# Kernel optimization log

Hardware: AMD Instinct MI355X
Metric: run time of the kernel (lower is better)

The kernel has to match this reference:

```python
import jax, jax.numpy as jnp
import numpy as np

N_NODES = 100000
N_EDGES = 1600000
N_FEAT = 128
HIDDEN = 64
NUM_GRAPHS = 64


def setup_inputs() -> dict:
    key = jax.random.key(0)
    ks = jax.random.split(key, 10)
    x = jax.random.normal(ks[0], (N_NODES, N_FEAT), dtype=jnp.float32)
    W = jax.random.normal(ks[1], (N_FEAT, HIDDEN), dtype=jnp.float32) * (1.0 / np.sqrt(N_FEAT))
    b = jax.random.normal(ks[2], (HIDDEN,), dtype=jnp.float32) * 0.01
    W1 = jax.random.normal(ks[3], (HIDDEN, 16), dtype=jnp.float32) * (1.0 / np.sqrt(HIDDEN))
    b1 = jax.random.normal(ks[4], (16,), dtype=jnp.float32) * 0.01
    W2 = jax.random.normal(ks[5], (16, 1), dtype=jnp.float32) * 0.25
    b2 = jax.random.normal(ks[6], (1,), dtype=jnp.float32) * 0.01
    edge_index = jax.random.randint(ks[7], (2, N_EDGES), 0, N_NODES, dtype=jnp.int64)
    batch = jnp.sort(jax.random.randint(ks[8], (N_NODES,), 0, NUM_GRAPHS, dtype=jnp.int64))
    return {"x": x, "W": W, "b": b, "W1": W1, "b1": b1, "W2": W2, "b2": b2,
            "edge_index": edge_index, "batch": batch, "num_graphs": NUM_GRAPHS}


def reference(x, W, b, W1, b1, W2, b2, edge_index, batch, num_graphs):
    N = x.shape[0]
    # GCNConv: h = D^-1/2 (A + I) D^-1/2 (x W) + b
    h = x @ W  # [N, H]
    loops = jnp.arange(N, dtype=edge_index.dtype)
    src = jnp.concatenate([edge_index[0], loops])  # source nodes (with self-loops)
    dst = jnp.concatenate([edge_index[1], loops])  # target nodes
    deg = jax.ops.segment_sum(jnp.ones(dst.shape, h.dtype), dst, num_segments=N)
    dis = jnp.where(deg > 0, jax.lax.rsqrt(deg), 0.0)  # deg^-1/2, 0 for isolated
    norm = dis[src] * dis[dst]  # [E+N]
    msg = h[src] * norm[:, None]  # gather + normalize
    agg = jax.ops.segment_sum(msg, dst, num_segments=N) + b  # scatter-add + bias
    hn = jax.nn.relu(agg)
    # global_add_pool over graphs
    u = jax.ops.segment_sum(hn, batch, num_segments=num_graphs)  # [G, H]
    out = jax.nn.relu(u @ W1 + b1) @ W2 + b2  # [G, 1]
    return out.reshape(-1)
```

## Files before the change

kernel.cpp:

```cpp
#include <hip/hip_runtime.h>

#define N_NODES   100000
#define N_FEAT    128
#define N_EDGES   1600000
#define HIDDEN    64
#define NUM_GRAPHS 64
#define CHUNK   4096
#define NCHUNK  ((N_EDGES + CHUNK - 1) / CHUNK)
#define BSHIFT  8
#define NBUCKET ((N_NODES + 255) >> 8)
#define OFFS_W  (NBUCKET + 1)
#define CAP     4800
#define QE      ((CAP + 511) / 512)
#define WT_BLOCKS 4
#define GEMM_GRID ((N_NODES + 127) / 128)
#define AGG_NODES 64
#define AGG_BLOCKS ((N_NODES + AGG_NODES - 1) / AGG_NODES)

typedef unsigned int  uint32;
typedef unsigned short ushort16;

typedef __attribute__((ext_vector_type(8))) __bf16 bf16x8;
typedef __attribute__((ext_vector_type(4))) float  f32x4;
union Frag8 { bf16x8 v; unsigned short s[8]; uint4 q; };

static __device__ __forceinline__ unsigned short f2bf(float f) {
    uint32 u = __float_as_uint(f);
    u += 0x7fffu + ((u >> 16) & 1u);
    return (unsigned short)(u >> 16);
}

static __device__ __forceinline__ int scan512(int v, int t, int* wsum) {
    const int lane = t & 63;
    const int wv   = t >> 6;
#pragma unroll
    for (int off = 1; off < 64; off <<= 1) {
        const int n = __shfl_up(v, off);
        if (lane >= off) v += n;
    }
    if (lane == 63) wsum[wv] = v;
    __syncthreads();
    if (t < 8) {
        int s = wsum[t];
#pragma unroll
        for (int off = 1; off < 8; off <<= 1) {
            const int n = __shfl_up(s, off);
            if (t >= off) s += n;
        }
        wsum[t] = s;
    }
    __syncthreads();
    if (wv > 0) v += wsum[wv - 1];
    return v;
}

static __device__ __forceinline__ int scan256(int v, int t, int* wsum) {
    const int lane = t & 63;
    const int wv   = t >> 6;
#pragma unroll
    for (int off = 1; off < 64; off <<= 1) {
        const int n = __shfl_up(v, off);
        if (lane >= off) v += n;
    }
    if (lane == 63 && wv < 4) wsum[wv] = v;
    __syncthreads();
    if (t < 4) {
        int s = wsum[t];
#pragma unroll
        for (int off = 1; off < 4; off <<= 1) {
            const int n = __shfl_up(s, off);
            if (t >= off) s += n;
        }
        wsum[t] = s;
    }
    __syncthreads();
    if (wv > 0 && wv < 4) v += wsum[wv - 1];
    return v;
}

__global__ __launch_bounds__(512) void k_pre(const float* __restrict__ W,
                                             ushort16* __restrict__ Wt,
                                             const int* __restrict__ ei,
                                             int* __restrict__ src_out,
                                             unsigned char* __restrict__ dst8,
                                             int* __restrict__ offs) {
    __shared__ int hist[512];
    __shared__ int excl[512];
    __shared__ int wsum[8];
    __shared__ int ssrc[CHUNK];
    __shared__ int sdst[CHUNK];

    if (blockIdx.x < WT_BLOCKS) {
        const int base = blockIdx.x * 2048 + threadIdx.x;
#pragma unroll
        for (int j = 0; j < 4; ++j) {
            const int idx = base + j * 512;
            const int k = idx >> 6, n = idx & 63;
            Wt[n * N_FEAT + k] = f2bf(W[idx]);
        }
        return;
    }

    const int c = blockIdx.x - WT_BLOCKS;
    const int base = c * CHUNK;
    const int n = min(CHUNK, N_EDGES - base);
    const int t = threadIdx.x;
    hist[t] = 0;
    __syncthreads();

    int es[CHUNK / 512], ed[CHUNK / 512], rk[CHUNK / 512];
#pragma unroll
    for (int k = 0; k < CHUNK / 512; ++k) {
        const int i = t + k * 512;
        if (i < n) {
            ed[k] = __builtin_nontemporal_load(&ei[N_EDGES + base + i]);
            es[k] = __builtin_nontemporal_load(&ei[base + i]);
            rk[k] = atomicAdd(&hist[ed[k] >> BSHIFT], 1);
        }
    }
    __syncthreads();

    const int cnt = hist[t];
    const int inc = scan512(cnt, t, wsum);
    excl[t] = inc - cnt;
    __syncthreads();
    if (t <= NBUCKET) offs[c * OFFS_W + t] = base + excl[t];

#pragma unroll
    for (int k = 0; k < CHUNK / 512; ++k) {
        const int i = t + k * 512;
        if (i < n) {
            const int pos = excl[ed[k] >> BSHIFT] + rk[k];
            ssrc[pos] = es[k];
            sdst[pos] = ed[k];
        }
    }
    __syncthreads();

    for (int i = t; i < n; i += 512)
        src_out[base + i] = ssrc[i];
    for (int i = t * 4; i < n; i += 2048) {
        const uint32 p = (uint32)(sdst[i] & 255)
                       | ((uint32)(sdst[i + 1] & 255) << 8)
                       | ((uint32)(sdst[i + 2] & 255) << 16)
                       | ((uint32)(sdst[i + 3] & 255) << 24);
        *(uint32*)&dst8[base + i] = p;
    }
}

__global__ __launch_bounds__(512) void k_mix(const float* __restrict__ x,
                                             const ushort16* __restrict__ Wt,
                                             ushort16* __restrict__ hb,
                                             const int* __restrict__ offs,
                                             const int* __restrict__ src_tmp,
                                             const unsigned char* __restrict__ dst8,
                                             int* __restrict__ srcs,
                                             int* __restrict__ row_ptr,
                                             int* __restrict__ row_end,
                                             float* __restrict__ dis) {
    __shared__ int hist[256];
    __shared__ int nxt[256];
    __shared__ int segb[NCHUNK];
    __shared__ int pre[NCHUNK + 1];
    __shared__ unsigned short cmap[CAP];
    __shared__ int ssrc[CAP];
    __shared__ int wsum[8];
    __shared__ int sb;

    if (blockIdx.x >= NBUCKET) {
        const int t    = threadIdx.x;
        const int lane = t & 63;
        const int wv   = t >> 6;
        const int m15  = lane & 15;
        const int quad = lane >> 4;
        const int base = (blockIdx.x - NBUCKET) * 128 + wv * 16;
        const int arow = min(base + m15, N_NODES - 1);

        const float* xr = &x[(size_t)arow * N_FEAT + quad * 8];
        float4 xa[4][2];
#pragma unroll
        for (int kc = 0; kc < 4; ++kc) {
            xa[kc][0] = *(const float4*)&xr[kc * 32];
            xa[kc][1] = *(const float4*)&xr[kc * 32 + 4];
        }

        Frag8 bfr[4][4];
#pragma unroll
        for (int nt = 0; nt < 4; ++nt) {
            const ushort16* wr = &Wt[(nt * 16 + m15) * N_FEAT + quad * 8];
#pragma unroll
            for (int kc = 0; kc < 4; ++kc)
                bfr[nt][kc].q = *(const uint4*)&wr[kc * 32];
        }

        Frag8 af[4];
#pragma unroll
        for (int kc = 0; kc < 4; ++kc) {
            const float* f = (const float*)&xa[kc][0];
#pragma unroll
            for (int j = 0; j < 8; ++j) af[kc].s[j] = f2bf(f[j]);
        }

        f32x4 acc[4];
#pragma unroll
        for (int nt = 0; nt < 4; ++nt) acc[nt] = (f32x4){0.f, 0.f, 0.f, 0.f};

#pragma unroll
        for (int kc = 0; kc < 4; ++kc)
#pragma unroll
            for (int nt = 0; nt < 4; ++nt)
                acc[nt] = __builtin_amdgcn_mfma_f32_16x16x32_bf16(af[kc].v, bfr[nt][kc].v,
                                                                  acc[nt], 0, 0, 0);

#pragma unroll
        for (int r = 0; r < 4; ++r) {
            const int orow = base + quad * 4 + r;
            if (orow < N_NODES) {
#pragma unroll
                for (int nt = 0; nt < 4; ++nt)
                    hb[(size_t)orow * HIDDEN + nt * 16 + m15] = f2bf(acc[nt][r]);
            }
        }
        return;
    }

    const int b = blockIdx.x;
    const int lo = b << BSHIFT;
    const int t = threadIdx.x;

    if (t < 256) hist[t] = 0;
    if (t == 0) sb = 0;
    __syncthreads();

    int len = 0;
    if (t < NCHUNK) {
        const int s0 = offs[t * OFFS_W + b];
        const int s1 = offs[t * OFFS_W + b + 1];
        segb[t] = s0;
        len = s1 - s0;
        atomicAdd(&sb, s0 - t * CHUNK);
    }
    const int inc = scan512(len, t, wsum);
    if (t == 0) pre[0] = 0;
    if (t < NCHUNK) pre[t + 1] = inc;
    __syncthreads();

    const int total  = pre[NCHUNK];
    const int bstart = sb;
    const bool fits  = (total <= CAP);

    int es[QE], ed[QE], rk[QE];
    if (fits) {
        if (t < NCHUNK) {
            const int p0 = pre[t], p1 = pre[t + 1];
            for (int j = p0; j < p1; ++j) cmap[j] = (unsigned short)t;
        }
        __syncthreads();
#pragma unroll
        for (int q = 0; q < QE; ++q) {
            const int e = t + q * 512;
            if (e < total) {
                const int c2 = cmap[e];
                const int gidx = segb[c2] + (e - pre[c2]);
                ed[q] = dst8[gidx];
                es[q] = src_tmp[gidx];
                rk[q] = atomicAdd(&hist[ed[q]], 1);
            }
        }
    } else {
        const int lane = t & 63, wv = t >> 6;
        for (int c2 = wv; c2 < NCHUNK; c2 += 8)
            for (int i = segb[c2] + lane; i < segb[c2] + (pre[c2 + 1] - pre[c2]); i += 64)
                atomicAdd(&hist[dst8[i]], 1);
    }
    __syncthreads();

    const int cv  = (t < 256) ? hist[t] : 0;
    const int hin = scan256(cv, t, wsum);
    if (t < 256) {
        const int excl = hin - cv;
        nxt[t] = excl;
        const int node = lo + t;
        if (node < N_NODES) {
            row_ptr[node] = bstart + excl;
            row_end[node] = bstart + excl + cv;
            dis[node]     = rsqrtf((float)cv + 1.0f);
        }
    }
    __syncthreads();

    if (fits) {
#pragma unroll
        for (int q = 0; q < QE; ++q)
            if (t + q * 512 < total) ssrc[nxt[ed[q]] + rk[q]] = es[q];
        __syncthreads();
        for (int i = t; i < total; i += 512)
            srcs[bstart + i] = ssrc[i];
    } else {
        const int lane = t & 63, wv = t >> 6;
        for (int c2 = wv; c2 < NCHUNK; c2 += 8)
            for (int i = segb[c2] + lane; i < segb[c2] + (pre[c2 + 1] - pre[c2]); i += 64) {
                const int d = dst8[i];
                const int pos = atomicAdd(&nxt[d], 1);
                srcs[bstart + pos] = src_tmp[i];
            }
    }
}

__global__ __launch_bounds__(256) void k_agg(const int* __restrict__ rp_g,
                                             const int* __restrict__ re_g,
                                             const int* __restrict__ srcs,
                                             const ushort16* __restrict__ hb,
                                             const float* __restrict__ dis,
                                             const float* __restrict__ bias,
                                             const int* __restrict__ batch,
                                             float* __restrict__ u) {
    __shared__ float sp[AGG_NODES * 65];
    __shared__ int   rp[AGG_NODES];
    __shared__ int   rc[AGG_NODES];
    __shared__ float sdn[AGG_NODES];
    __shared__ int   gbs[AGG_NODES];
    const int b  = blockIdx.x;
    const int lo = b * AGG_NODES;
    const int t  = threadIdx.x;

    if (t < AGG_NODES) {
        const int node = lo + t;
        const bool ok = node < N_NODES;
        const int p = ok ? rp_g[node] : 0;
        rp[t]  = p;
        rc[t]  = ok ? (re_g[node] - p) : 0;
        sdn[t] = ok ? dis[node] : 0.f;
        gbs[t] = ok ? batch[node] : 0;
    }
    __syncthreads();

    const int lane = t & 63;
    const int k    = lane & 7;
    const int kb   = lane & 56;
    const int grp  = (t >> 6) * 8 + (lane >> 3);

    float acc[2][8];
#pragma unroll
    for (int a = 0; a < 2; ++a)
#pragma unroll
        for (int j = 0; j < 8; ++j) acc[a][j] = 0.f;

#pragma unroll
    for (int a = 0; a < 2; ++a) {
        const int n   = grp * 2 + a;
        const int beg = rp[n];
        const int L   = rc[n];
        for (int i = 0; i < L; i += 8) {
            const int idx = beg + min(i + k, L - 1);
            const int sv  = srcs[idx];
            const float wv_ = dis[sv];
            uint4 v[8];
            float w[8];
#pragma unroll
            for (int j = 0; j < 8; ++j) {
                const int sj = __shfl(sv, kb | j);
                w[j] = __shfl(wv_, kb | j);
                v[j] = *(const uint4*)&hb[(size_t)sj * HIDDEN + k * 8];
            }
            const int rem = L - i;
#pragma unroll
            for (int j = 0; j < 8; ++j) {
                const float m = (j < rem) ? w[j] : 0.f;
                acc[a][0] = fmaf(__uint_as_float(v[j].x << 16),         m, acc[a][0]);
                acc[a][1] = fmaf(__uint_as_float(v[j].x & 0xffff0000u), m, acc[a][1]);
                acc[a][2] = fmaf(__uint_as_float(v[j].y << 16),         m, acc[a][2]);
                acc[a][3] = fmaf(__uint_as_float(v[j].y & 0xffff0000u), m, acc[a][3]);
                acc[a][4] = fmaf(__uint_as_float(v[j].z << 16),         m, acc[a][4]);
                acc[a][5] = fmaf(__uint_as_float(v[j].z & 0xffff0000u), m, acc[a][5]);
                acc[a][6] = fmaf(__uint_as_float(v[j].w << 16),         m, acc[a][6]);
                acc[a][7] = fmaf(__uint_as_float(v[j].w & 0xffff0000u), m, acc[a][7]);
            }
        }
    }

    const float4 b0 = *(const float4*)&bias[k * 8];
    const float4 b1 = *(const float4*)&bias[k * 8 + 4];
#pragma unroll
    for (int a = 0; a < 2; ++a) {
        const int n = grp * 2 + a;
        const uint4 hv = *(const uint4*)
            &hb[(size_t)min(lo + n, N_NODES - 1) * HIDDEN + k * 8];
        const float dn = sdn[n];
        float4 r0, r1;
        r0.x = fmaxf(fmaf(fmaf(__uint_as_float(hv.x << 16),         dn, acc[a][0]), dn, b0.x), 0.f);
        r0.y = fmaxf(fmaf(fmaf(__uint_as_float(hv.x & 0xffff0000u), dn, acc[a][1]), dn, b0.y), 0.f);
        r0.z = fmaxf(fmaf(fmaf(__uint_as_float(hv.y << 16),         dn, acc[a][2]), dn, b0.z), 0.f);
        r0.w = fmaxf(fmaf(fmaf(__uint_as_float(hv.y & 0xffff0000u), dn, acc[a][3]), dn, b0.w), 0.f);
        r1.x = fmaxf(fmaf(fmaf(__uint_as_float(hv.z << 16),         dn, acc[a][4]), dn, b1.x), 0.f);
        r1.y = fmaxf(fmaf(fmaf(__uint_as_float(hv.z & 0xffff0000u), dn, acc[a][5]), dn, b1.y), 0.f);
        r1.z = fmaxf(fmaf(fmaf(__uint_as_float(hv.w << 16),         dn, acc[a][6]), dn, b1.z), 0.f);
        r1.w = fmaxf(fmaf(fmaf(__uint_as_float(hv.w & 0xffff0000u), dn, acc[a][7]), dn, b1.w), 0.f);
        *(float4*)&sp[n * 65 + k * 8]     = r0;
        *(float4*)&sp[n * 65 + k * 8 + 4] = r1;
    }
    __syncthreads();

    const int f   = t & 63;
    const int seg = t >> 6;
    float a_ = 0.f;
    int   cg = -1;
    for (int n2 = seg * 16; n2 < seg * 16 + 16; ++n2) {
        const int node = lo + n2;
        if (node >= N_NODES) break;
        const float r = sp[n2 * 65 + f];
        const int gr = gbs[n2];
        if (gr != cg) {
            if (cg >= 0) atomicAdd(&u[cg * HIDDEN + f], a_);
            cg = gr; a_ = r;
        } else {
            a_ += r;
        }
    }
    if (cg >= 0) atomicAdd(&u[cg * HIDDEN + f], a_);
}

__global__ __launch_bounds__(64) void mlp_kernel(const float* __restrict__ u,
                                                 const float* __restrict__ W1,
                                                 const float* __restrict__ b1,
                                                 const float* __restrict__ W2,
                                                 const float* __restrict__ b2,
                                                 float* __restrict__ out) {
    __shared__ float W1s[HIDDEN * 16];
    __shared__ float W2s[16];
    __shared__ float b1s[16];
    const int t = threadIdx.x;
    for (int i = t; i < HIDDEN * 16; i += 64) W1s[i] = W1[i];
    if (t < 16) { W2s[t] = W2[t]; b1s[t] = b1[t]; }
    __syncthreads();
    if (t < NUM_GRAPHS) {
        float uu[HIDDEN];
#pragma unroll
        for (int k = 0; k < HIDDEN; ++k) uu[k] = u[t * HIDDEN + k];
        float o = b2[0];
#pragma unroll
        for (int j = 0; j < 16; ++j) {
            float s = b1s[j];
#pragma unroll
            for (int k = 0; k < HIDDEN; ++k) s = fmaf(uu[k], W1s[k * 16 + j], s);
            o = fmaf(fmaxf(s, 0.f), W2s[j], o);
        }
        out[t] = o;
    }
}

extern "C" void kernel_launch(void* const* d_in, const int* in_sizes, int n_in,
                              void* d_out, int out_size, void* d_ws, size_t ws_size,
                              hipStream_t stream) {
    const float* x  = (const float*)d_in[0];
    const float* W  = (const float*)d_in[1];
    const float* b  = (const float*)d_in[2];
    const float* W1 = (const float*)d_in[3];
    const float* b1 = (const float*)d_in[4];
    const float* W2 = (const float*)d_in[5];
    const float* b2 = (const float*)d_in[6];
    const int*   ei = (const int*)d_in[7];
    const int* batch = (const int*)d_in[8];
    float* out = (float*)d_out;

    ushort16* hb       = (ushort16*)d_ws;
    int*      src_tmp  = (int*)(hb + (size_t)N_NODES * HIDDEN);
    unsigned char* dst8 = (unsigned char*)(src_tmp + N_EDGES);
    int*      srcs     = (int*)(dst8 + N_EDGES);
    int*      offs     = srcs + N_EDGES;
    int*      row_ptr  = offs + NCHUNK * OFFS_W;
    int*      row_end  = row_ptr + N_NODES;
    float*    dis      = (float*)(row_end + N_NODES);
    float*    u        = dis + N_NODES;
    ushort16* Wtg      = (ushort16*)(u + NUM_GRAPHS * HIDDEN);

    hipMemsetAsync(u, 0, NUM_GRAPHS * HIDDEN * sizeof(float), stream);

    k_pre<<<WT_BLOCKS + NCHUNK, 512, 0, stream>>>(W, Wtg, ei, src_tmp, dst8, offs);
    k_mix<<<NBUCKET + GEMM_GRID, 512, 0, stream>>>(x, Wtg, hb, offs, src_tmp, dst8,
                                                   srcs, row_ptr, row_end, dis);
    k_agg<<<AGG_BLOCKS, 256, 0, stream>>>(row_ptr, row_end, srcs, hb, dis, b, batch, u);
    mlp_kernel<<<1, 64, 0, stream>>>(u, W1, b1, W2, b2, out);
}
```

Baseline: 177.3 us.

## Fuse CSR bucket sort into aggregation kernel and drop global srcs/row_ptr

Moves the per-bucket counting sort of edges from k_mix into k_agg, so each 512-thread aggregation block sorts its 256-node bucket's edges in shared memory (in CAP-sized passes) and aggregates directly from the LDS-resident source list. k_mix now only computes the degree histogram and dis. This removes the global srcs/row_ptr/row_end writes and reads. The memset of u is folded into k_pre. The trade-off is a much larger, heavier k_agg with fewer blocks (one per bucket), multiple sync-heavy passes, and serial per-chunk histogram loops in k_mix, which may reduce parallelism and occupancy.

```diff
diff --git a/kernel.cpp b/kernel.cpp
--- a/kernel.cpp
+++ b/kernel.cpp
@@ -14,8 +14,6 @@
 #define QE      ((CAP + 511) / 512)
 #define WT_BLOCKS 4
 #define GEMM_GRID ((N_NODES + 127) / 128)
-#define AGG_NODES 64
-#define AGG_BLOCKS ((N_NODES + AGG_NODES - 1) / AGG_NODES)
 
 typedef unsigned int  uint32;
 typedef unsigned short ushort16;
@@ -83,7 +81,8 @@
                                              const int* __restrict__ ei,
                                              int* __restrict__ src_out,
                                              unsigned char* __restrict__ dst8,
-                                             int* __restrict__ offs) {
+                                             int* __restrict__ offs,
+                                             float* __restrict__ u) {
     __shared__ int hist[512];
     __shared__ int excl[512];
     __shared__ int wsum[8];
@@ -98,6 +97,9 @@
             const int k = idx >> 6, n = idx & 63;
             Wt[n * N_FEAT + k] = f2bf(W[idx]);
         }
+        if (blockIdx.x == 0)
+            for (int i = threadIdx.x; i < NUM_GRAPHS * HIDDEN; i += 512)
+                u[i] = 0.f;
         return;
     }
 
@@ -152,20 +154,9 @@
                                              const ushort16* __restrict__ Wt,
                                              ushort16* __restrict__ hb,
                                              const int* __restrict__ offs,
-                                             const int* __restrict__ src_tmp,
                                              const unsigned char* __restrict__ dst8,
-                                             int* __restrict__ srcs,
-                                             int* __restrict__ row_ptr,
-                                             int* __restrict__ row_end,
                                              float* __restrict__ dis) {
     __shared__ int hist[256];
-    __shared__ int nxt[256];
-    __shared__ int segb[NCHUNK];
-    __shared__ int pre[NCHUNK + 1];
-    __shared__ unsigned short cmap[CAP];
-    __shared__ int ssrc[CAP];
-    __shared__ int wsum[8];
-    __shared__ int sb;
 
     if (blockIdx.x >= NBUCKET) {
         const int t    = threadIdx.x;
@@ -224,200 +215,203 @@
         return;
     }
 
-    const int b = blockIdx.x;
+    const int b  = blockIdx.x;
     const int lo = b << BSHIFT;
-    const int t = threadIdx.x;
-
+    const int t  = threadIdx.x;
     if (t < 256) hist[t] = 0;
-    if (t == 0) sb = 0;
-    __syncthreads();
-
-    int len = 0;
+    __syncthreads();
+
     if (t < NCHUNK) {
         const int s0 = offs[t * OFFS_W + b];
         const int s1 = offs[t * OFFS_W + b + 1];
-        segb[t] = s0;
-        len = s1 - s0;
-        atomicAdd(&sb, s0 - t * CHUNK);
-    }
-    const int inc = scan512(len, t, wsum);
-    if (t == 0) pre[0] = 0;
-    if (t < NCHUNK) pre[t + 1] = inc;
-    __syncthreads();
-
-    const int total  = pre[NCHUNK];
-    const int bstart = sb;
-    const bool fits  = (total <= CAP);
-
-    int es[QE], ed[QE], rk[QE];
-    if (fits) {
-        if (t < NCHUNK) {
-            const int p0 = pre[t], p1 = pre[t + 1];
-            for (int j = p0; j < p1; ++j) cmap[j] = (unsigned short)t;
-        }
-        __syncthreads();
-#pragma unroll
-        for (int q = 0; q < QE; ++q) {
-            const int e = t + q * 512;
-            if (e < total) {
-                const int c2 = cmap[e];
-                const int gidx = segb[c2] + (e - pre[c2]);
-                ed[q] = dst8[gidx];
-                es[q] = src_tmp[gidx];
-                rk[q] = atomicAdd(&hist[ed[q]], 1);
-            }
-        }
-    } else {
-        const int lane = t & 63, wv = t >> 6;
-        for (int c2 = wv; c2 < NCHUNK; c2 += 8)
-            for (int i = segb[c2] + lane; i < segb[c2] + (pre[c2 + 1] - pre[c2]); i += 64)
-                atomicAdd(&hist[dst8[i]], 1);
-    }
-    __syncthreads();
-
-    const int cv  = (t < 256) ? hist[t] : 0;
-    const int hin = scan256(cv, t, wsum);
+        for (int i = s0; i < s1; ++i)
+            atomicAdd(&hist[dst8[i]], 1);
+    }
+    __syncthreads();
+
     if (t < 256) {
-        const int excl = hin - cv;
-        nxt[t] = excl;
         const int node = lo + t;
-        if (node < N_NODES) {
-            row_ptr[node] = bstart + excl;
-            row_end[node] = bstart + excl + cv;
-            dis[node]     = rsqrtf((float)cv + 1.0f);
-        }
-    }
-    __syncthreads();
-
-    if (fits) {
-#pragma unroll
-        for (int q = 0; q < QE; ++q)
-            if (t + q * 512 < total) ssrc[nxt[ed[q]] + rk[q]] = es[q];
-        __syncthreads();
-        for (int i = t; i < total; i += 512)
-            srcs[bstart + i] = ssrc[i];
-    } else {
-        const int lane = t & 63, wv = t >> 6;
-        for (int c2 = wv; c2 < NCHUNK; c2 += 8)
-            for (int i = segb[c2] + lane; i < segb[c2] + (pre[c2 + 1] - pre[c2]); i += 64) {
-                const int d = dst8[i];
-                const int pos = atomicAdd(&nxt[d], 1);
-                srcs[bstart + pos] = src_tmp[i];
-            }
-    }
-}
-
-__global__ __launch_bounds__(256) void k_agg(const int* __restrict__ rp_g,
-                                             const int* __restrict__ re_g,
-                                             const int* __restrict__ srcs,
+        if (node < N_NODES)
+            dis[node] = rsqrtf((float)hist[t] + 1.f);
+    }
+}
+
+__global__ __launch_bounds__(512) void k_agg(const int* __restrict__ offs,
+                                             const int* __restrict__ src_tmp,
+                                             const unsigned char* __restrict__ dst8,
                                              const ushort16* __restrict__ hb,
                                              const float* __restrict__ dis,
                                              const float* __restrict__ bias,
                                              const int* __restrict__ batch,
                                              float* __restrict__ u) {
-    __shared__ float sp[AGG_NODES * 65];
-    __shared__ int   rp[AGG_NODES];
-    __shared__ int   rc[AGG_NODES];
-    __shared__ float sdn[AGG_NODES];
-    __shared__ int   gbs[AGG_NODES];
+    __shared__ __align__(16) char arena[33280];
+    __shared__ int   segb[NCHUNK];
+    __shared__ int   pre[NCHUNK + 1];
+    __shared__ int   hist[256];
+    __shared__ int   nxt[256];
+    __shared__ int   cnt_s[256];
+    __shared__ float sdn[256];
+    __shared__ int   gbs[256];
+    __shared__ int   wsum[8];
+    __shared__ int   c1s;
+    unsigned short* cmap = (unsigned short*)arena;
+    int*   ssrc = (int*)(arena + 9728);
+    float* sp   = (float*)arena;
+
     const int b  = blockIdx.x;
-    const int lo = b * AGG_NODES;
+    const int lo = b << BSHIFT;
     const int t  = threadIdx.x;
 
-    if (t < AGG_NODES) {
+    int len = 0;
+    if (t < NCHUNK) {
+        const int s0 = offs[t * OFFS_W + b];
+        segb[t] = s0;
+        len = offs[t * OFFS_W + b + 1] - s0;
+    }
+    if (t < 256) {
         const int node = lo + t;
         const bool ok = node < N_NODES;
-        const int p = ok ? rp_g[node] : 0;
-        rp[t]  = p;
-        rc[t]  = ok ? (re_g[node] - p) : 0;
         sdn[t] = ok ? dis[node] : 0.f;
         gbs[t] = ok ? batch[node] : 0;
     }
-    __syncthreads();
-
-    const int lane = t & 63;
-    const int k    = lane & 7;
-    const int kb   = lane & 56;
-    const int grp  = (t >> 6) * 8 + (lane >> 3);
-
-    float acc[2][8];
-#pragma unroll
-    for (int a = 0; a < 2; ++a)
+    const int inc = scan512(len, t, wsum);
+    if (t == 0) { pre[0] = 0; c1s = 0; }
+    if (t < NCHUNK) pre[t + 1] = inc;
+    __syncthreads();
+
+    const int total = pre[NCHUNK];
+    const int lane  = t & 63;
+    const int k     = lane & 7;
+    const int kb    = lane & 56;
+    const int grp   = (t >> 6) * 8 + (lane >> 3);
+
+    float acc[4][8];
+#pragma unroll
+    for (int a = 0; a < 4; ++a)
 #pragma unroll
         for (int j = 0; j < 8; ++j) acc[a][j] = 0.f;
 
-#pragma unroll
-    for (int a = 0; a < 2; ++a) {
-        const int n   = grp * 2 + a;
-        const int beg = rp[n];
-        const int L   = rc[n];
-        for (int i = 0; i < L; i += 8) {
-            const int idx = beg + min(i + k, L - 1);
-            const int sv  = srcs[idx];
-            const float wv_ = dis[sv];
-            uint4 v[8];
-            float w[8];
-#pragma unroll
-            for (int j = 0; j < 8; ++j) {
-                const int sj = __shfl(sv, kb | j);
-                w[j] = __shfl(wv_, kb | j);
-                v[j] = *(const uint4*)&hb[(size_t)sj * HIDDEN + k * 8];
+    int c0 = 0, e0 = 0;
+    while (e0 < total) {
+        if (t <= NCHUNK && pre[t] <= e0 + CAP) atomicMax(&c1s, t);
+        if (t < 256) hist[t] = 0;
+        __syncthreads();
+        const int c1 = c1s;
+        const int e1 = pre[c1];
+        const int Tp = e1 - e0;
+
+        if (t >= c0 && t < c1) {
+            const int p0 = pre[t] - e0, p1 = pre[t + 1] - e0;
+            for (int j = p0; j < p1; ++j) cmap[j] = (unsigned short)t;
+        }
+        __syncthreads();
+
+        int es[QE], ed[QE], rk[QE];
+#pragma unroll
+        for (int q = 0; q < QE; ++q) {
+            const int e = t + q * 512;
+            if (e < Tp) {
+                const int c2 = cmap[e];
+                const int gidx = segb[c2] + (e + e0 - pre[c2]);
+                ed[q] = dst8[gidx];
+                es[q] = src_tmp[gidx];
+                rk[q] = atomicAdd(&hist[ed[q]], 1);
             }
-            const int rem = L - i;
-#pragma unroll
-            for (int j = 0; j < 8; ++j) {
-                const float m = (j < rem) ? w[j] : 0.f;
-                acc[a][0] = fmaf(__uint_as_float(v[j].x << 16),         m, acc[a][0]);
-                acc[a][1] = fmaf(__uint_as_float(v[j].x & 0xffff0000u), m, acc[a][1]);
-                acc[a][2] = fmaf(__uint_as_float(v[j].y << 16),         m, acc[a][2]);
-                acc[a][3] = fmaf(__uint_as_float(v[j].y & 0xffff0000u), m, acc[a][3]);
-                acc[a][4] = fmaf(__uint_as_float(v[j].z << 16),         m, acc[a][4]);
-                acc[a][5] = fmaf(__uint_as_float(v[j].z & 0xffff0000u), m, acc[a][5]);
-                acc[a][6] = fmaf(__uint_as_float(v[j].w << 16),         m, acc[a][6]);
-                acc[a][7] = fmaf(__uint_as_float(v[j].w & 0xffff0000u), m, acc[a][7]);
+        }
+        __syncthreads();
+
+        const int cv  = (t < 256) ? hist[t] : 0;
+        const int hin = scan256(cv, t, wsum);
+        if (t < 256) { nxt[t] = hin - cv; cnt_s[t] = cv; }
+        if (t == 0) c1s = 0;
+        __syncthreads();
+
+#pragma unroll
+        for (int q = 0; q < QE; ++q)
+            if (t + q * 512 < Tp) ssrc[nxt[ed[q]] + rk[q]] = es[q];
+        __syncthreads();
+
+#pragma unroll
+        for (int a = 0; a < 4; ++a) {
+            const int n   = grp * 4 + a;
+            const int beg = nxt[n];
+            const int L   = cnt_s[n];
+            for (int i = 0; i < L; i += 8) {
+                const int sv  = ssrc[beg + min(i + k, L - 1)];
+                const float wv_ = dis[sv];
+                uint4 v[8];
+                float w[8];
+#pragma unroll
+                for (int j = 0; j < 8; ++j) {
+                    const int sj = __shfl(sv, kb | j);
+                    w[j] = __shfl(wv_, kb | j);
+                    v[j] = *(const uint4*)&hb[(size_t)sj * HIDDEN + k * 8];
+                }
+                const int rem = L - i;
+#pragma unroll
+                for (int j = 0; j < 8; ++j) {
+                    const float m = (j < rem) ? w[j] : 0.f;
+                    acc[a][0] = fmaf(__uint_as_float(v[j].x << 16),         m, acc[a][0]);
+                    acc[a][1] = fmaf(__uint_as_float(v[j].x & 0xffff0000u), m, acc[a][1]);
+                    acc[a][2] = fmaf(__uint_as_float(v[j].y << 16),         m, acc[a][2]);
+                    acc[a][3] = fmaf(__uint_as_float(v[j].y & 0xffff0000u), m, acc[a][3]);
+                    acc[a][4] = fmaf(__uint_as_float(v[j].z << 16),         m, acc[a][4]);
+                    acc[a][5] = fmaf(__uint_as_float(v[j].z & 0xffff0000u), m, acc[a][5]);
+                    acc[a][6] = fmaf(__uint_as_float(v[j].w << 16),         m, acc[a][6]);
+                    acc[a][7] = fmaf(__uint_as_float(v[j].w & 0xffff0000u), m, acc[a][7]);
+                }
             }
         }
+        __syncthreads();
+        c0 = c1; e0 = e1;
     }
 
     const float4 b0 = *(const float4*)&bias[k * 8];
     const float4 b1 = *(const float4*)&bias[k * 8 + 4];
-#pragma unroll
-    for (int a = 0; a < 2; ++a) {
-        const int n = grp * 2 + a;
-        const uint4 hv = *(const uint4*)
-            &hb[(size_t)min(lo + n, N_NODES - 1) * HIDDEN + k * 8];
-        const float dn = sdn[n];
-        float4 r0, r1;
-        r0.x = fmaxf(fmaf(fmaf(__uint_as_float(hv.x << 16),         dn, acc[a][0]), dn, b0.x), 0.f);
-        r0.y = fmaxf(fmaf(fmaf(__uint_as_float(hv.x & 0xffff0000u), dn, acc[a][1]), dn, b0.y), 0.f);
-        r0.z = fmaxf(fmaf(fmaf(__uint_as_float(hv.y << 16),         dn, acc[a][2]), dn, b0.z), 0.f);
-        r0.w = fmaxf(fmaf(fmaf(__uint_as_float(hv.y & 0xffff0000u), dn, acc[a][3]), dn, b0.w), 0.f);
-        r1.x = fmaxf(fmaf(fmaf(__uint_as_float(hv.z << 16),         dn, acc[a][4]), dn, b1.x), 0.f);
-        r1.y = fmaxf(fmaf(fmaf(__uint_as_float(hv.z & 0xffff0000u), dn, acc[a][5]), dn, b1.y), 0.f);
-        r1.z = fmaxf(fmaf(fmaf(__uint_as_float(hv.w << 16),         dn, acc[a][6]), dn, b1.z), 0.f);
-        r1.w = fmaxf(fmaf(fmaf(__uint_as_float(hv.w & 0xffff0000u), dn, acc[a][7]), dn, b1.w), 0.f);
-        *(float4*)&sp[n * 65 + k * 8]     = r0;
-        *(float4*)&sp[n * 65 + k * 8 + 4] = r1;
-    }
-    __syncthreads();
-
     const int f   = t & 63;
     const int seg = t >> 6;
-    float a_ = 0.f;
-    int   cg = -1;
-    for (int n2 = seg * 16; n2 < seg * 16 + 16; ++n2) {
-        const int node = lo + n2;
-        if (node >= N_NODES) break;
-        const float r = sp[n2 * 65 + f];
-        const int gr = gbs[n2];
-        if (gr != cg) {
-            if (cg >= 0) atomicAdd(&u[cg * HIDDEN + f], a_);
-            cg = gr; a_ = r;
-        } else {
-            a_ += r;
-        }
-    }
-    if (cg >= 0) atomicAdd(&u[cg * HIDDEN + f], a_);
+
+    for (int h = 0; h < 2; ++h) {
+        if ((grp >> 5) == h) {
+#pragma unroll
+            for (int a = 0; a < 4; ++a) {
+                const int n  = grp * 4 + a;
+                const int nl = n - h * 128;
+                const uint4 hv = *(const uint4*)
+                    &hb[(size_t)min(lo + n, N_NODES - 1) * HIDDEN + k * 8];
+                const float dn = sdn[n];
+                float4 r0, r1;
+                r0.x = fmaxf(fmaf(fmaf(__uint_as_float(hv.x << 16),         dn, acc[a][0]), dn, b0.x), 0.f);
+                r0.y = fmaxf(fmaf(fmaf(__uint_as_float(hv.x & 0xffff0000u), dn, acc[a][1]), dn, b0.y), 0.f);
+                r0.z = fmaxf(fmaf(fmaf(__uint_as_float(hv.y << 16),         dn, acc[a][2]), dn, b0.z), 0.f);
+                r0.w = fmaxf(fmaf(fmaf(__uint_as_float(hv.y & 0xffff0000u), dn, acc[a][3]), dn, b0.w), 0.f);
+                r1.x = fmaxf(fmaf(fmaf(__uint_as_float(hv.z << 16),         dn, acc[a][4]), dn, b1.x), 0.f);
+                r1.y = fmaxf(fmaf(fmaf(__uint_as_float(hv.z & 0xffff0000u), dn, acc[a][5]), dn, b1.y), 0.f);
+                r1.z = fmaxf(fmaf(fmaf(__uint_as_float(hv.w << 16),         dn, acc[a][6]), dn, b1.z), 0.f);
+                r1.w = fmaxf(fmaf(fmaf(__uint_as_float(hv.w & 0xffff0000u), dn, acc[a][7]), dn, b1.w), 0.f);
+                *(float4*)&sp[nl * 65 + k * 8]     = r0;
+                *(float4*)&sp[nl * 65 + k * 8 + 4] = r1;
+            }
+        }
+        __syncthreads();
+
+        float a_ = 0.f;
+        int   cg = -1;
+        for (int n2 = seg * 16; n2 < seg * 16 + 16; ++n2) {
+            const int node = lo + h * 128 + n2;
+            if (node >= N_NODES) break;
+            const float r = sp[n2 * 65 + f];
+            const int gr = gbs[h * 128 + n2];
+            if (gr != cg) {
+                if (cg >= 0) atomicAdd(&u[cg * HIDDEN + f], a_);
+                cg = gr; a_ = r;
+            } else {
+                a_ += r;
+            }
+        }
+        if (cg >= 0) atomicAdd(&u[cg * HIDDEN + f], a_);
+        __syncthreads();
+    }
 }
 
 __global__ __launch_bounds__(64) void mlp_kernel(const float* __restrict__ u,
@@ -466,19 +460,13 @@
     ushort16* hb       = (ushort16*)d_ws;
     int*      src_tmp  = (int*)(hb + (size_t)N_NODES * HIDDEN);
     unsigned char* dst8 = (unsigned char*)(src_tmp + N_EDGES);
-    int*      srcs     = (int*)(dst8 + N_EDGES);
-    int*      offs     = srcs + N_EDGES;
-    int*      row_ptr  = offs + NCHUNK * OFFS_W;
-    int*      row_end  = row_ptr + N_NODES;
-    float*    dis      = (float*)(row_end + N_NODES);
+    int*      offs     = (int*)(dst8 + N_EDGES);
+    float*    dis      = (float*)(offs + NCHUNK * OFFS_W);
     float*    u        = dis + N_NODES;
     ushort16* Wtg      = (ushort16*)(u + NUM_GRAPHS * HIDDEN);
 
-    hipMemsetAsync(u, 0, NUM_GRAPHS * HIDDEN * sizeof(float), stream);
-
-    k_pre<<<WT_BLOCKS + NCHUNK, 512, 0, stream>>>(W, Wtg, ei, src_tmp, dst8, offs);
-    k_mix<<<NBUCKET + GEMM_GRID, 512, 0, stream>>>(x, Wtg, hb, offs, src_tmp, dst8,
-                                                   srcs, row_ptr, row_end, dis);
-    k_agg<<<AGG_BLOCKS, 256, 0, stream>>>(row_ptr, row_end, srcs, hb, dis, b, batch, u);
+    k_pre<<<WT_BLOCKS + NCHUNK, 512, 0, stream>>>(W, Wtg, ei, src_tmp, dst8, offs, u);
+    k_mix<<<NBUCKET + GEMM_GRID, 512, 0, stream>>>(x, Wtg, hb, offs, dst8, dis);
+    k_agg<<<NBUCKET, 512, 0, stream>>>(offs, src_tmp, dst8, hb, dis, b, batch, u);
     mlp_kernel<<<1, 64, 0, stream>>>(u, W1, b1, W2, b2, out);
 }
```

Result: slower. 204.3 us (+15.2%).
